# Kernel optimization log

Hardware: AMD Instinct MI355X
Metric: run time of the kernel (lower is better)

## Reference

```python
import jax, jax.numpy as jnp
import numpy as np

WEIGHT = 1.0
TEMPERATURE = 1.0
POWER = 2.0
NEG_FILL = -1e9
EPS = 1e-8


def _cos_sim_matrix(x):
    # row-normalize then GEMM: equivalent to pairwise F.cosine_similarity
    norms = jnp.linalg.norm(x, axis=-1, keepdims=True)
    xn = x / jnp.maximum(norms, EPS)
    return xn @ xn.T  # [N, N]


def setup_inputs() -> dict:
    key = jax.random.key(0)
    k1, k2 = jax.random.split(key)
    model_output = jax.random.normal(k1, (8192, 512), dtype=jnp.float32)
    targets = jax.random.normal(k2, (8192, 768), dtype=jnp.float32)
    return {"model_output": model_output, "targets": targets}


def reference(model_output, targets):
    N = model_output.shape[0]
    eye = jnp.eye(N, dtype=bool)

    sim_o = jnp.where(eye, NEG_FILL, _cos_sim_matrix(model_output))
    sim_t = jnp.where(eye, NEG_FILL, _cos_sim_matrix(targets))

    student_log_probs = jax.nn.log_softmax(sim_o / TEMPERATURE, axis=-1)
    teacher_probs = jax.nn.softmax(sim_t / TEMPERATURE, axis=-1)

    weights = jax.lax.stop_gradient(teacher_probs ** POWER)

    # torch F.kl_div(input=log_p_student, target=p_teacher, reduction='none')
    # = where(target > 0, target * (log(target) - input), 0)
    tp_safe = jnp.where(teacher_probs > 0, teacher_probs, 1.0)
    kl = jnp.where(teacher_probs > 0,
                   teacher_probs * (jnp.log(tp_safe) - student_log_probs),
                   0.0)

    loss = jnp.mean(weights * kl)
    return WEIGHT * loss
```

## Files before the change

kernel.cpp:

```cpp
#include <hip/hip_runtime.h>

#define N    8192
#define DT   768
#define DO   512
#define BM   128
#define BN   128
#define TI   (N / BM)
#define TJ   (N / BN)
#define NTILE (TI * (TI + 1) / 2)
#define NSLOT (2 * TJ)
#define PL    ((size_t)NSLOT * N)
#define NKT   (DT / 32)
#define NKO   (DO / 32)

typedef __attribute__((ext_vector_type(8))) short   short8;
typedef __attribute__((ext_vector_type(4))) float   floatx4;

struct alignas(8) us4 { unsigned short x[4]; };

__device__ inline unsigned short f2bf(float x) {
    union { float f; unsigned int u; } v; v.f = x;
    unsigned int r = v.u + 0x7fffu + ((v.u >> 16) & 1u);
    return (unsigned short)(r >> 16);
}
__device__ inline float bf2f(unsigned short u) {
    union { unsigned int u; float f; } v; v.u = ((unsigned int)u) << 16;
    return v.f;
}

__device__ inline void gl2lds16(const unsigned short* g, unsigned short* l) {
    __builtin_amdgcn_global_load_lds(
        (const __attribute__((address_space(1))) unsigned int*)(const void*)g,
        (__attribute__((address_space(3))) unsigned int*)(void*)l,
        16, 0, 0);
}

template <int D>
__device__ inline void stage_tile(const unsigned short* __restrict__ X,
                                  unsigned short* sAb, unsigned short* sBb,
                                  int i0, int j0, int k, int t) {
    #pragma unroll
    for (int h = 0; h < 2; ++h) {
        const int idx = t + h * 256;
        const int r   = idx >> 2;
        const int cs  = ((idx & 3) ^ ((r >> 1) & 3)) << 3;
        gl2lds16(X + (size_t)(i0 + r) * D + k + cs, &sAb[idx * 8]);
        gl2lds16(X + (size_t)(j0 + r) * D + k + cs, &sBb[idx * 8]);
    }
}

__device__ inline void mfma_step(const unsigned short* __restrict__ sAb,
                                 const unsigned short* __restrict__ sBb,
                                 floatx4 (&acc)[4][4],
                                 int wm, int wn, int lr, int lgx) {
    short8 af[4], bf[4];
    #pragma unroll
    for (int mi = 0; mi < 4; ++mi)
        af[mi] = *(const short8*)&sAb[(wm * 64 + mi * 16 + lr) * 32 + (lgx << 3)];
    #pragma unroll
    for (int ni = 0; ni < 4; ++ni)
        bf[ni] = *(const short8*)&sBb[(wn * 64 + ni * 16 + lr) * 32 + (lgx << 3)];
    #pragma unroll
    for (int mi = 0; mi < 4; ++mi)
        #pragma unroll
        for (int ni = 0; ni < 4; ++ni)
            acc[mi][ni] = __builtin_amdgcn_mfma_f32_16x16x32_bf16(
                af[mi], bf[ni], acc[mi][ni], 0, 0, 0);
}

__device__ inline void tile_coords(int bid, int& ti, int& tj) {
    int swb = (bid & 7) * (NTILE / 8) + (bid >> 3);
    int sti = 0, stj = 0;
    for (;;) {
        const int sz = (sti == stj) ? 36 : 64;
        if (swb < sz) break;
        swb -= sz;
        if (++stj == 8) { ++sti; stj = sti; }
    }
    int i, j;
    if (sti == stj) {
        i = 0;
        while (swb >= 8 - i) { swb -= 8 - i; ++i; }
        j = i + swb;
    } else {
        i = swb >> 3;
        j = swb & 7;
    }
    ti = sti * 8 + i;
    tj = stj * 8 + j;
}

__global__ void norm_kernel(const float* __restrict__ Tg,
                            const float* __restrict__ Mo,
                            unsigned short* __restrict__ Xt,
                            unsigned short* __restrict__ Xo,
                            float* __restrict__ zero_me) {
    if (blockIdx.x == 0 && threadIdx.x == 0) zero_me[0] = 0.0f;
    int bid = blockIdx.x;
    const float* X; unsigned short* Xn; int D;
    if (bid < N / 4) { X = Tg; Xn = Xt; D = DT; }
    else             { bid -= N / 4; X = Mo; Xn = Xo; D = DO; }
    const int row  = bid * 4 + (threadIdx.x >> 6);
    const int lane = threadIdx.x & 63;
    const int nch  = D >> 8;
    const float* xr = X + (size_t)row * D;
    floatx4 vc[3];
    float ss = 0.0f;
    #pragma unroll
    for (int h = 0; h < 3; ++h) {
        if (h < nch) {
            vc[h] = *(const floatx4*)(xr + lane * 4 + h * 256);
            ss += vc[h][0] * vc[h][0] + vc[h][1] * vc[h][1]
                + vc[h][2] * vc[h][2] + vc[h][3] * vc[h][3];
        }
    }
    #pragma unroll
    for (int m = 32; m >= 1; m >>= 1) ss += __shfl_xor(ss, m);
    const float scale = 1.0f / fmaxf(sqrtf(ss), 1e-8f);
    unsigned short* outr = Xn + (size_t)row * D;
    #pragma unroll
    for (int h = 0; h < 3; ++h) {
        if (h < nch) {
            us4 o;
            #pragma unroll
            for (int j = 0; j < 4; ++j) o.x[j] = f2bf(vc[h][j] * scale);
            *(us4*)(outr + lane * 4 + h * 256) = o;
        }
    }
}

__launch_bounds__(256, 3)
__global__ void fused_t_kernel(const unsigned short* __restrict__ Xt,
                               float* __restrict__ partials,
                               unsigned int* __restrict__ Wws) {
    __shared__ unsigned short sA[3][BM * 32];
    __shared__ unsigned short sB[3][BN * 32];

    const int t    = threadIdx.x;
    const int lane = t & 63;
    const int w    = t >> 6;
    const int wm   = w >> 1, wn = w & 1;
    const int lr   = lane & 15, lg = lane >> 4;
    const int lgx  = lg ^ ((lr >> 1) & 3);

    int ti, tj; tile_coords(blockIdx.x, ti, tj);
    const bool offdiag = (ti != tj);
    const int i0 = ti * BM, j0 = tj * BN;
    unsigned int* const wt = Wws + (size_t)blockIdx.x * 8192;

    floatx4 acc[4][4];
    #pragma unroll
    for (int a = 0; a < 4; ++a)
        #pragma unroll
        for (int b = 0; b < 4; ++b)
            acc[a][b] = (floatx4){0.0f, 0.0f, 0.0f, 0.0f};

    stage_tile<DT>(Xt, sA[0], sB[0], i0, j0, 0, t);
    stage_tile<DT>(Xt, sA[1], sB[1], i0, j0, 32, t);

    for (int s = 0; s < NKT; ++s) {
        if (s + 1 < NKT) asm volatile("s_waitcnt vmcnt(4)" ::: "memory");
        else             asm volatile("s_waitcnt vmcnt(0)" ::: "memory");
        __builtin_amdgcn_s_barrier();
        asm volatile("" ::: "memory");
        if (s + 2 < NKT)
            stage_tile<DT>(Xt, sA[(s + 2) % 3], sB[(s + 2) % 3], i0, j0, (s + 2) * 32, t);
        mfma_step(sA[s % 3], sB[s % 3], acc, wm, wn, lr, lgx);
        asm volatile("" ::: "memory");
    }

    {
        float czt[4], cvv[4], cua[4];
        #pragma unroll
        for (int ni = 0; ni < 4; ++ni) { czt[ni] = 0.0f; cvv[ni] = 0.0f; cua[ni] = 0.0f; }
        #pragma unroll
        for (int mi = 0; mi < 4; ++mi) {
            unsigned int wpk[4][2];
            #pragma unroll
            for (int r = 0; r < 4; ++r) {
                const int row = wm * 64 + mi * 16 + lg * 4 + r;
                const int gi  = i0 + row;
                float zt = 0.0f, vv = 0.0f, ua = 0.0f;
                #pragma unroll
                for (int ni = 0; ni < 4; ++ni) {
                    const int gj = j0 + wn * 64 + ni * 16 + lr;
                    const float a = acc[mi][ni][r];
                    float ea = __expf(a - 1.0f);
                    if (gi == gj) ea = 0.0f;
                    const float e3 = ea * ea * ea;
                    zt += ea; vv += e3; ua += e3 * a;
                    czt[ni] += ea; cvv[ni] += e3; cua[ni] += e3 * a;
                    if ((r & 1) == 0) wpk[ni][r >> 1]  = (unsigned int)f2bf(e3);
                    else              wpk[ni][r >> 1] |= ((unsigned int)f2bf(e3)) << 16;
                }
                #pragma unroll
                for (int m = 8; m >= 1; m >>= 1) {
                    zt += __shfl_xor(zt, m);
                    vv += __shfl_xor(vv, m);
                    ua += __shfl_xor(ua, m);
                }
                if (lr == 0) {
                    const size_t base = (size_t)(tj * 2 + wn) * N + gi;
                    partials[0 * PL + base] = zt;
                    partials[1 * PL + base] = vv;
                    partials[2 * PL + base] = ua;
                }
            }
            #pragma unroll
            for (int ni = 0; ni < 4; ++ni)
                #pragma unroll
                for (int rp = 0; rp < 2; ++rp)
                    wt[(mi * 8 + ni * 2 + rp) * 256 + t] = wpk[ni][rp];
        }
        if (offdiag) {
            #pragma unroll
            for (int ni = 0; ni < 4; ++ni) {
                #pragma unroll
                for (int m = 16; m <= 32; m <<= 1) {
                    czt[ni] += __shfl_xor(czt[ni], m);
                    cvv[ni] += __shfl_xor(cvv[ni], m);
                    cua[ni] += __shfl_xor(cua[ni], m);
                }
            }
            if (lg == 0) {
                #pragma unroll
                for (int ni = 0; ni < 4; ++ni) {
                    const int gj = j0 + wn * 64 + ni * 16 + lr;
                    const size_t base = (size_t)(ti * 2 + wm) * N + gj;
                    partials[0 * PL + base] = czt[ni];
                    partials[1 * PL + base] = cvv[ni];
                    partials[2 * PL + base] = cua[ni];
                }
            }
        }
    }
}

__launch_bounds__(256, 3)
__global__ void fused_o_kernel(const unsigned short* __restrict__ Xo,
                               float* __restrict__ partials,
                               const unsigned int* __restrict__ Wws) {
    __shared__ unsigned short sA[3][BM * 32];
    __shared__ unsigned short sB[3][BN * 32];

    const int t    = threadIdx.x;
    const int lane = t & 63;
    const int w    = t >> 6;
    const int wm   = w >> 1, wn = w & 1;
    const int lr   = lane & 15, lg = lane >> 4;
    const int lgx  = lg ^ ((lr >> 1) & 3);

    int ti, tj; tile_coords(blockIdx.x, ti, tj);
    const bool offdiag = (ti != tj);
    const int i0 = ti * BM, j0 = tj * BN;
    const unsigned int* const wt = Wws + (size_t)blockIdx.x * 8192;

    floatx4 acc[4][4];
    #pragma unroll
    for (int a = 0; a < 4; ++a)
        #pragma unroll
        for (int b = 0; b < 4; ++b)
            acc[a][b] = (floatx4){0.0f, 0.0f, 0.0f, 0.0f};

    stage_tile<DO>(Xo, sA[0], sB[0], i0, j0, 0, t);
    stage_tile<DO>(Xo, sA[1], sB[1], i0, j0, 32, t);

    for (int s = 0; s < NKO; ++s) {
        if (s + 1 < NKO) asm volatile("s_waitcnt vmcnt(4)" ::: "memory");
        else             asm volatile("s_waitcnt vmcnt(0)" ::: "memory");
        __builtin_amdgcn_s_barrier();
        asm volatile("" ::: "memory");
        if (s + 2 < NKO)
            stage_tile<DO>(Xo, sA[(s + 2) % 3], sB[(s + 2) % 3], i0, j0, (s + 2) * 32, t);
        mfma_step(sA[s % 3], sB[s % 3], acc, wm, wn, lr, lgx);
        asm volatile("" ::: "memory");
    }

    {
        unsigned int wld[32];
        #pragma unroll
        for (int pi = 0; pi < 32; ++pi)
            wld[pi] = wt[pi * 256 + t];
        float czo[4], cwb[4];
        #pragma unroll
        for (int ni = 0; ni < 4; ++ni) { czo[ni] = 0.0f; cwb[ni] = 0.0f; }
        #pragma unroll
        for (int mi = 0; mi < 4; ++mi) {
            #pragma unroll
            for (int r = 0; r < 4; ++r) {
                const int row = wm * 64 + mi * 16 + lg * 4 + r;
                const int gi  = i0 + row;
                float zo = 0.0f, wb = 0.0f;
                #pragma unroll
                for (int ni = 0; ni < 4; ++ni) {
                    const int gj = j0 + wn * 64 + ni * 16 + lr;
                    const float b = acc[mi][ni][r];
                    float eb = __expf(b - 1.0f);
                    if (gi == gj) eb = 0.0f;
                    const unsigned int pw = wld[mi * 8 + ni * 2 + (r >> 1)];
                    const float wgt = bf2f((unsigned short)((r & 1) ? (pw >> 16)
                                                                    : (pw & 0xffffu)));
                    zo += eb; wb += wgt * b;
                    czo[ni] += eb; cwb[ni] += wgt * b;
                }
                #pragma unroll
                for (int m = 8; m >= 1; m >>= 1) {
                    zo += __shfl_xor(zo, m);
                    wb += __shfl_xor(wb, m);
                }
                if (lr == 0) {
                    const size_t base = (size_t)(tj * 2 + wn) * N + gi;
                    partials[3 * PL + base] = zo;
                    partials[4 * PL + base] = wb;
                }
            }
        }
        if (offdiag) {
            #pragma unroll
            for (int ni = 0; ni < 4; ++ni) {
                #pragma unroll
                for (int m = 16; m <= 32; m <<= 1) {
                    czo[ni] += __shfl_xor(czo[ni], m);
                    cwb[ni] += __shfl_xor(cwb[ni], m);
                }
            }
            if (lg == 0) {
                #pragma unroll
                for (int ni = 0; ni < 4; ++ni) {
                    const int gj = j0 + wn * 64 + ni * 16 + lr;
                    const size_t base = (size_t)(ti * 2 + wm) * N + gj;
                    partials[3 * PL + base] = czo[ni];
                    partials[4 * PL + base] = cwb[ni];
                }
            }
        }
    }
}

__global__ void reduce_kernel(const float* __restrict__ partials,
                              float* __restrict__ out) {
    __shared__ float sh[5][256];
    const int t    = threadIdx.x;
    const int lane = t & 63;
    const int g    = t >> 6;
    const int i    = blockIdx.x * 64 + lane;
    float s[5] = {0.0f, 0.0f, 0.0f, 0.0f, 0.0f};
    for (int jb = g * (NSLOT / 4); jb < (g + 1) * (NSLOT / 4); ++jb) {
        const size_t base = (size_t)jb * N + i;
        #pragma unroll
        for (int p = 0; p < 5; ++p) s[p] += partials[p * PL + base];
    }
    #pragma unroll
    for (int p = 0; p < 5; ++p) sh[p][t] = s[p];
    __syncthreads();
    if (g == 0) {
        float v[5];
        #pragma unroll
        for (int p = 0; p < 5; ++p)
            v[p] = sh[p][lane] + sh[p][64 + lane] + sh[p][128 + lane] + sh[p][192 + lane];
        float li = (v[2] - v[4] + v[1] * __logf(v[3] / v[0])) / (v[0] * v[0] * v[0]);
        #pragma unroll
        for (int m = 32; m >= 1; m >>= 1) li += __shfl_xor(li, m);
        if (lane == 0)
            atomicAdd(out, li * (1.0f / ((float)N * (float)N)));
    }
}

extern "C" void kernel_launch(void* const* d_in, const int* in_sizes, int n_in,
                              void* d_out, int out_size, void* d_ws, size_t ws_size,
                              hipStream_t stream) {
    (void)in_sizes; (void)n_in; (void)out_size; (void)ws_size;
    const float* mo = (const float*)d_in[0];
    const float* tg = (const float*)d_in[1];
    float* out = (float*)d_out;

    char* ws = (char*)d_ws;
    unsigned short* Xt = (unsigned short*)ws;
    unsigned short* Xo = (unsigned short*)(ws + (size_t)N * DT * 2);
    float* partials    = (float*)(ws + (size_t)N * DT * 2 + (size_t)N * DO * 2);
    unsigned int* Wws  = (unsigned int*)((char*)partials + 5 * PL * sizeof(float));

    norm_kernel<<<2 * (N / 4), 256, 0, stream>>>(tg, mo, Xt, Xo, out);
    fused_t_kernel<<<NTILE, 256, 0, stream>>>(Xt, partials, Wws);
    fused_o_kernel<<<NTILE, 256, 0, stream>>>(Xo, partials, Wws);
    reduce_kernel<<<N / 64, 256, 0, stream>>>(partials, out);
}
```

Before: 320.9 us.

## Fuse teacher and student GEMM kernels, keep weights in LDS, drop triple buffering

Merges the two per-tile GEMM kernels into one kernel that computes the teacher tile, stores the bf16 cubed weights in shared memory, then computes the student tile on the same block. This removes the global workspace round trip for the weights and one kernel launch. In exchange the K loop loses its triple-buffered asynchronous prefetch and becomes a load, wait, compute loop with two barriers per step. The new 32 KB weight buffer in LDS also raises shared memory per block, which may lower occupancy.

```diff
diff --git a/kernel.cpp b/kernel.cpp
--- a/kernel.cpp
+++ b/kernel.cpp
@@ -10,8 +10,6 @@
 #define NTILE (TI * (TI + 1) / 2)
 #define NSLOT (2 * TJ)
 #define PL    ((size_t)NSLOT * N)
-#define NKT   (DT / 32)
-#define NKO   (DO / 32)
 
 typedef __attribute__((ext_vector_type(8))) short   short8;
 typedef __attribute__((ext_vector_type(4))) float   floatx4;
@@ -37,35 +35,16 @@
 
 template <int D>
 __device__ inline void stage_tile(const unsigned short* __restrict__ X,
-                                  unsigned short* sAb, unsigned short* sBb,
+                                  unsigned short* sA, unsigned short* sB,
                                   int i0, int j0, int k, int t) {
     #pragma unroll
     for (int h = 0; h < 2; ++h) {
         const int idx = t + h * 256;
         const int r   = idx >> 2;
         const int cs  = ((idx & 3) ^ ((r >> 1) & 3)) << 3;
-        gl2lds16(X + (size_t)(i0 + r) * D + k + cs, &sAb[idx * 8]);
-        gl2lds16(X + (size_t)(j0 + r) * D + k + cs, &sBb[idx * 8]);
-    }
-}
-
-__device__ inline void mfma_step(const unsigned short* __restrict__ sAb,
-                                 const unsigned short* __restrict__ sBb,
-                                 floatx4 (&acc)[4][4],
-                                 int wm, int wn, int lr, int lgx) {
-    short8 af[4], bf[4];
-    #pragma unroll
-    for (int mi = 0; mi < 4; ++mi)
-        af[mi] = *(const short8*)&sAb[(wm * 64 + mi * 16 + lr) * 32 + (lgx << 3)];
-    #pragma unroll
-    for (int ni = 0; ni < 4; ++ni)
-        bf[ni] = *(const short8*)&sBb[(wn * 64 + ni * 16 + lr) * 32 + (lgx << 3)];
-    #pragma unroll
-    for (int mi = 0; mi < 4; ++mi)
-        #pragma unroll
-        for (int ni = 0; ni < 4; ++ni)
-            acc[mi][ni] = __builtin_amdgcn_mfma_f32_16x16x32_bf16(
-                af[mi], bf[ni], acc[mi][ni], 0, 0, 0);
+        gl2lds16(X + (size_t)(i0 + r) * D + k + cs, &sA[idx * 8]);
+        gl2lds16(X + (size_t)(j0 + r) * D + k + cs, &sB[idx * 8]);
+    }
 }
 
 __device__ inline void tile_coords(int bid, int& ti, int& tj) {
@@ -130,11 +109,12 @@
 }
 
 __launch_bounds__(256, 3)
-__global__ void fused_t_kernel(const unsigned short* __restrict__ Xt,
-                               float* __restrict__ partials,
-                               unsigned int* __restrict__ Wws) {
-    __shared__ unsigned short sA[3][BM * 32];
-    __shared__ unsigned short sB[3][BN * 32];
+__global__ void fused_kernel(const unsigned short* __restrict__ Xt,
+                             const unsigned short* __restrict__ Xo,
+                             float* __restrict__ partials) {
+    __shared__ unsigned short sA[BM * 32];
+    __shared__ unsigned short sB[BN * 32];
+    __shared__ unsigned short sW[64 * 256];
 
     const int t    = threadIdx.x;
     const int lane = t & 63;
@@ -146,7 +126,6 @@
     int ti, tj; tile_coords(blockIdx.x, ti, tj);
     const bool offdiag = (ti != tj);
     const int i0 = ti * BM, j0 = tj * BN;
-    unsigned int* const wt = Wws + (size_t)blockIdx.x * 8192;
 
     floatx4 acc[4][4];
     #pragma unroll
@@ -155,18 +134,24 @@
         for (int b = 0; b < 4; ++b)
             acc[a][b] = (floatx4){0.0f, 0.0f, 0.0f, 0.0f};
 
-    stage_tile<DT>(Xt, sA[0], sB[0], i0, j0, 0, t);
-    stage_tile<DT>(Xt, sA[1], sB[1], i0, j0, 32, t);
-
-    for (int s = 0; s < NKT; ++s) {
-        if (s + 1 < NKT) asm volatile("s_waitcnt vmcnt(4)" ::: "memory");
-        else             asm volatile("s_waitcnt vmcnt(0)" ::: "memory");
-        __builtin_amdgcn_s_barrier();
-        asm volatile("" ::: "memory");
-        if (s + 2 < NKT)
-            stage_tile<DT>(Xt, sA[(s + 2) % 3], sB[(s + 2) % 3], i0, j0, (s + 2) * 32, t);
-        mfma_step(sA[s % 3], sB[s % 3], acc, wm, wn, lr, lgx);
-        asm volatile("" ::: "memory");
+    for (int k = 0; k < DT; k += 32) {
+        stage_tile<DT>(Xt, sA, sB, i0, j0, k, t);
+        asm volatile("s_waitcnt vmcnt(0)" ::: "memory");
+        __syncthreads();
+        short8 af[4], bf[4];
+        #pragma unroll
+        for (int mi = 0; mi < 4; ++mi)
+            af[mi] = *(const short8*)&sA[(wm * 64 + mi * 16 + lr) * 32 + (lgx << 3)];
+        #pragma unroll
+        for (int ni = 0; ni < 4; ++ni)
+            bf[ni] = *(const short8*)&sB[(wn * 64 + ni * 16 + lr) * 32 + (lgx << 3)];
+        #pragma unroll
+        for (int mi = 0; mi < 4; ++mi)
+            #pragma unroll
+            for (int ni = 0; ni < 4; ++ni)
+                acc[mi][ni] = __builtin_amdgcn_mfma_f32_16x16x32_bf16(
+                    af[mi], bf[ni], acc[mi][ni], 0, 0, 0);
+        __syncthreads();
     }
 
     {
@@ -175,7 +160,6 @@
         for (int ni = 0; ni < 4; ++ni) { czt[ni] = 0.0f; cvv[ni] = 0.0f; cua[ni] = 0.0f; }
         #pragma unroll
         for (int mi = 0; mi < 4; ++mi) {
-            unsigned int wpk[4][2];
             #pragma unroll
             for (int r = 0; r < 4; ++r) {
                 const int row = wm * 64 + mi * 16 + lg * 4 + r;
@@ -190,8 +174,7 @@
                     const float e3 = ea * ea * ea;
                     zt += ea; vv += e3; ua += e3 * a;
                     czt[ni] += ea; cvv[ni] += e3; cua[ni] += e3 * a;
-                    if ((r & 1) == 0) wpk[ni][r >> 1]  = (unsigned int)f2bf(e3);
-                    else              wpk[ni][r >> 1] |= ((unsigned int)f2bf(e3)) << 16;
+                    sW[(mi * 16 + ni * 4 + r) * 256 + t] = f2bf(e3);
                 }
                 #pragma unroll
                 for (int m = 8; m >= 1; m >>= 1) {
@@ -206,11 +189,6 @@
                     partials[2 * PL + base] = ua;
                 }
             }
-            #pragma unroll
-            for (int ni = 0; ni < 4; ++ni)
-                #pragma unroll
-                for (int rp = 0; rp < 2; ++rp)
-                    wt[(mi * 8 + ni * 2 + rp) * 256 + t] = wpk[ni][rp];
         }
         if (offdiag) {
             #pragma unroll
@@ -234,53 +212,34 @@
             }
         }
     }
-}
-
-__launch_bounds__(256, 3)
-__global__ void fused_o_kernel(const unsigned short* __restrict__ Xo,
-                               float* __restrict__ partials,
-                               const unsigned int* __restrict__ Wws) {
-    __shared__ unsigned short sA[3][BM * 32];
-    __shared__ unsigned short sB[3][BN * 32];
-
-    const int t    = threadIdx.x;
-    const int lane = t & 63;
-    const int w    = t >> 6;
-    const int wm   = w >> 1, wn = w & 1;
-    const int lr   = lane & 15, lg = lane >> 4;
-    const int lgx  = lg ^ ((lr >> 1) & 3);
-
-    int ti, tj; tile_coords(blockIdx.x, ti, tj);
-    const bool offdiag = (ti != tj);
-    const int i0 = ti * BM, j0 = tj * BN;
-    const unsigned int* const wt = Wws + (size_t)blockIdx.x * 8192;
-
-    floatx4 acc[4][4];
+
     #pragma unroll
     for (int a = 0; a < 4; ++a)
         #pragma unroll
         for (int b = 0; b < 4; ++b)
             acc[a][b] = (floatx4){0.0f, 0.0f, 0.0f, 0.0f};
 
-    stage_tile<DO>(Xo, sA[0], sB[0], i0, j0, 0, t);
-    stage_tile<DO>(Xo, sA[1], sB[1], i0, j0, 32, t);
-
-    for (int s = 0; s < NKO; ++s) {
-        if (s + 1 < NKO) asm volatile("s_waitcnt vmcnt(4)" ::: "memory");
-        else             asm volatile("s_waitcnt vmcnt(0)" ::: "memory");
-        __builtin_amdgcn_s_barrier();
-        asm volatile("" ::: "memory");
-        if (s + 2 < NKO)
-            stage_tile<DO>(Xo, sA[(s + 2) % 3], sB[(s + 2) % 3], i0, j0, (s + 2) * 32, t);
-        mfma_step(sA[s % 3], sB[s % 3], acc, wm, wn, lr, lgx);
-        asm volatile("" ::: "memory");
+    for (int k = 0; k < DO; k += 32) {
+        stage_tile<DO>(Xo, sA, sB, i0, j0, k, t);
+        asm volatile("s_waitcnt vmcnt(0)" ::: "memory");
+        __syncthreads();
+        short8 af[4], bf[4];
+        #pragma unroll
+        for (int mi = 0; mi < 4; ++mi)
+            af[mi] = *(const short8*)&sA[(wm * 64 + mi * 16 + lr) * 32 + (lgx << 3)];
+        #pragma unroll
+        for (int ni = 0; ni < 4; ++ni)
+            bf[ni] = *(const short8*)&sB[(wn * 64 + ni * 16 + lr) * 32 + (lgx << 3)];
+        #pragma unroll
+        for (int mi = 0; mi < 4; ++mi)
+            #pragma unroll
+            for (int ni = 0; ni < 4; ++ni)
+                acc[mi][ni] = __builtin_amdgcn_mfma_f32_16x16x32_bf16(
+                    af[mi], bf[ni], acc[mi][ni], 0, 0, 0);
+        __syncthreads();
     }
 
     {
-        unsigned int wld[32];
-        #pragma unroll
-        for (int pi = 0; pi < 32; ++pi)
-            wld[pi] = wt[pi * 256 + t];
         float czo[4], cwb[4];
         #pragma unroll
         for (int ni = 0; ni < 4; ++ni) { czo[ni] = 0.0f; cwb[ni] = 0.0f; }
@@ -297,9 +256,7 @@
                     const float b = acc[mi][ni][r];
                     float eb = __expf(b - 1.0f);
                     if (gi == gj) eb = 0.0f;
-                    const unsigned int pw = wld[mi * 8 + ni * 2 + (r >> 1)];
-                    const float wgt = bf2f((unsigned short)((r & 1) ? (pw >> 16)
-                                                                    : (pw & 0xffffu)));
+                    const float wgt = bf2f(sW[(mi * 16 + ni * 4 + r) * 256 + t]);
                     zo += eb; wb += wgt * b;
                     czo[ni] += eb; cwb[ni] += wgt * b;
                 }
@@ -378,10 +335,8 @@
     unsigned short* Xt = (unsigned short*)ws;
     unsigned short* Xo = (unsigned short*)(ws + (size_t)N * DT * 2);
     float* partials    = (float*)(ws + (size_t)N * DT * 2 + (size_t)N * DO * 2);
-    unsigned int* Wws  = (unsigned int*)((char*)partials + 5 * PL * sizeof(float));
 
     norm_kernel<<<2 * (N / 4), 256, 0, stream>>>(tg, mo, Xt, Xo, out);
-    fused_t_kernel<<<NTILE, 256, 0, stream>>>(Xt, partials, Wws);
-    fused_o_kernel<<<NTILE, 256, 0, stream>>>(Xo, partials, Wws);
+    fused_kernel<<<NTILE, 256, 0, stream>>>(Xt, Xo, partials);
     reduce_kernel<<<N / 64, 256, 0, stream>>>(partials, out);
 }
```

New measurement: 293.9 us. 1.09x faster.
